# Performance work log

Hardware: AMD Instinct MI355X
Metric: run time of the kernel (lower is better)

The kernel has to match this reference:

```python
import jax, jax.numpy as jnp
import numpy as np

N = 20000   # nodes
E = 320000  # edges
F0 = 32     # num_features
H = 8       # GAT heads
G = 64      # graphs in batch


def setup_inputs() -> dict:
    key = jax.random.key(0)
    ks = jax.random.split(key, 16)
    def p(k, shape, s=0.05):
        return jax.random.normal(k, shape, jnp.float32) * s
    d = {}
    d['x'] = jax.random.normal(ks[0], (N, F0), jnp.float32)
    d['edge_index'] = jax.random.randint(ks[1], (2, E), 0, N, dtype=jnp.int32)
    d['edge_weights'] = jax.random.uniform(ks[2], (E,), jnp.float32)
    d['batch'] = jnp.sort(jax.random.randint(ks[3], (N,), 0, G, dtype=jnp.int32))
    # GATConv(32 -> 32, heads=8)
    d['W_gat'] = p(ks[4], (F0, H * F0)); d['att_src'] = p(ks[5], (H, F0))
    d['att_dst'] = p(ks[6], (H, F0));    d['b_gat'] = jnp.zeros((H * F0,), jnp.float32)
    # residual Linear(256 -> 1024) (widened so the residual add is shape-consistent)
    d['W_res'] = p(ks[7], (H * F0, 1024)); d['b_res'] = jnp.zeros((1024,), jnp.float32)
    # GCNConv(256 -> 512) + BN1
    d['W2'] = p(ks[8], (H * F0, 512)); d['b2'] = jnp.zeros((512,), jnp.float32)
    d['g1'] = jnp.ones((512,), jnp.float32); d['be1'] = jnp.zeros((512,), jnp.float32)
    d['m1'] = jnp.zeros((512,), jnp.float32); d['v1'] = jnp.ones((512,), jnp.float32)
    # GCNConv(512 -> 1024) + BN2
    d['W3'] = p(ks[9], (512, 1024)); d['b3'] = jnp.zeros((1024,), jnp.float32)
    d['g2'] = jnp.ones((1024,), jnp.float32); d['be2'] = jnp.zeros((1024,), jnp.float32)
    d['m2'] = jnp.zeros((1024,), jnp.float32); d['v2'] = jnp.ones((1024,), jnp.float32)
    # head
    d['Wf1'] = p(ks[10], (1024, 256)); d['bf1'] = jnp.zeros((256,), jnp.float32)
    d['Wf2'] = p(ks[11], (256, 2));    d['bf2'] = jnp.zeros((2,), jnp.float32)
    return d


def _add_self_loops(edge_index, edge_weight, n):
    loop = jnp.arange(n, dtype=edge_index.dtype)
    ei = jnp.concatenate([edge_index, jnp.stack([loop, loop])], axis=1)
    ew = jnp.concatenate([edge_weight, jnp.ones((n,), edge_weight.dtype)])
    return ei, ew


def _gat(x, edge_index, W, att_src, att_dst, b, n):
    # PyG GATConv, concat=True, eval (attention dropout off). Self-loops already added.
    src, dst = edge_index[0], edge_index[1]
    h = (x @ W).reshape(n, H, -1)                    # [N,H,C]
    a_s = jnp.einsum('nhc,hc->nh', h, att_src)        # [N,H]
    a_d = jnp.einsum('nhc,hc->nh', h, att_dst)
    e = jax.nn.leaky_relu(a_s[src] + a_d[dst], 0.2)   # [E,H]
    m = jax.ops.segment_max(e, dst, num_segments=n)   # softmax over incoming edges
    ex = jnp.exp(e - m[dst])
    s = jax.ops.segment_sum(ex, dst, num_segments=n)
    alpha = ex / s[dst]
    out = jax.ops.segment_sum(h[src] * alpha[:, :, None], dst, num_segments=n)
    return out.reshape(n, -1) + b                     # [N,H*C]


def _gcn(x, edge_index, w, W, b, n):
    # PyG GCNConv with symmetric normalization; self-loops (weight 1) already added.
    src, dst = edge_index[0], edge_index[1]
    deg = jax.ops.segment_sum(w, dst, num_segments=n)
    dinv = jnp.where(deg > 0, jax.lax.rsqrt(jnp.maximum(deg, 1e-12)), 0.0)
    norm = dinv[src] * w * dinv[dst]                  # [E]
    h = x @ W                                         # transform first (cheaper)
    return jax.ops.segment_sum(h[src] * norm[:, None], dst, num_segments=n) + b


def _bn(x, g, b, m, v):
    return g * (x - m) * jax.lax.rsqrt(v + 1e-5) + b


def reference(x, edge_index, edge_weights, batch, W_gat, att_src, att_dst, b_gat,
              W_res, b_res, W2, b2, g1, be1, m1, v1, W3, b3, g2, be2, m2, v2,
              Wf1, bf1, Wf2, bf2):
    n = x.shape[0]
    ei, ew = _add_self_loops(edge_index, edge_weights, n)
    h = jax.nn.relu(_gat(x, ei, W_gat, att_src, att_dst, b_gat, n))   # [N,256]
    res = h @ W_res + b_res                                           # [N,1024]
    h = _gcn(h, ei, ew, W2, b2, n)                                    # [N,512]
    h = jax.nn.relu(_bn(h, g1, be1, m1, v1))
    h = _gcn(h, ei, ew, W3, b3, n)                                    # [N,1024]
    h = jax.nn.relu(_bn(h, g2, be2, m2, v2))
    h = h + res
    pooled = jax.ops.segment_max(h, batch, num_segments=G)            # global max pool [G,1024]
    z = jax.nn.relu(pooled @ Wf1 + bf1)                               # dropout is eval no-op
    return z @ Wf2 + bf2                                              # [G,2]
```

## Files before the change

kernel.cpp:

```cpp
#include <hip/hip_runtime.h>
#include <hip/hip_bf16.h>

#define NN 20000
#define EE 320000
#define GG 64
#define EN (EE + NN)
#define MT 157

typedef float f32x4 __attribute__((ext_vector_type(4)));
typedef __bf16 bf16x4 __attribute__((ext_vector_type(4)));
typedef __bf16 bf16x8 __attribute__((ext_vector_type(8)));

__global__ void sentinel_kernel(float* out, int n) {
    int i = blockIdx.x * 256 + threadIdx.x;
    if (i < n) out[i] = 12345.0f;
}

__global__ void init_kernel(int* deg_cnt, float* deg_w, int* fill, float* pooled) {
    int i = blockIdx.x * 256 + threadIdx.x;
    if (i < NN) { deg_cnt[i] = 1; deg_w[i] = 1.0f; fill[i] = 0; }
    if (i < GG * 1024) pooled[i] = -INFINITY;
}

__global__ void convert_wt(const float* __restrict__ W, __bf16* __restrict__ Wt, int K, int N) {
    int n = blockIdx.x;
    for (int k = threadIdx.x; k < K; k += 256)
        Wt[(size_t)n * K + k] = (__bf16)W[(size_t)k * N + n];
}

__global__ __launch_bounds__(256) void gat_transform(
    const float* __restrict__ x, const float* __restrict__ W,
    const float* __restrict__ att_s, const float* __restrict__ att_d,
    __bf16* __restrict__ hlin, float* __restrict__ a_s, float* __restrict__ a_d)
{
    __shared__ float Ws[32 * 256];
    int tid = threadIdx.x;
#pragma unroll
    for (int k = 0; k < 32; k++) Ws[k * 256 + tid] = W[k * 256 + tid];
    float asc = att_s[tid], adc = att_d[tid];
    __syncthreads();
    for (int n = blockIdx.x; n < NN; n += gridDim.x) {
        const float* xp = x + (size_t)n * 32;
        float acc = 0.f;
#pragma unroll
        for (int k = 0; k < 32; k++) acc += xp[k] * Ws[k * 256 + tid];
        hlin[(size_t)n * 256 + tid] = (__bf16)acc;
        float s = acc * asc, d = acc * adc;
#pragma unroll
        for (int m = 1; m <= 16; m <<= 1) { s += __shfl_xor(s, m); d += __shfl_xor(d, m); }
        if ((tid & 31) == 0) { int h = tid >> 5; a_s[n * 8 + h] = s; a_d[n * 8 + h] = d; }
    }
}

__global__ void deg_kernel(const int* __restrict__ ei, const float* __restrict__ ew,
                           int* deg_cnt, float* deg_w) {
    int e = blockIdx.x * 256 + threadIdx.x;
    if (e >= EE) return;
    int dst = ei[EE + e];
    atomicAdd(&deg_cnt[dst], 1);
    atomicAdd(&deg_w[dst], ew[e]);
}

__global__ void dinv_kernel(const float* __restrict__ deg_w, float* __restrict__ dinv) {
    int n = blockIdx.x * 256 + threadIdx.x;
    if (n < NN) dinv[n] = rsqrtf(deg_w[n]);
}

__global__ __launch_bounds__(256) void scan_kernel(const int* __restrict__ deg_cnt, int* __restrict__ rowptr) {
    __shared__ int partial[256];
    int tid = threadIdx.x;
    const int chunk = (NN + 255) / 256;
    int s0 = tid * chunk, s1 = min(s0 + chunk, NN);
    int sum = 0;
    for (int i = s0; i < s1; i++) sum += deg_cnt[i];
    partial[tid] = sum;
    __syncthreads();
    if (tid == 0) {
        int run = 0;
        for (int i = 0; i < 256; i++) { int t = partial[i]; partial[i] = run; run += t; }
        rowptr[NN] = run;
    }
    __syncthreads();
    int run = partial[tid];
    for (int i = s0; i < s1; i++) { rowptr[i] = run; run += deg_cnt[i]; }
}

__global__ void fill_kernel(const int* __restrict__ ei, const float* __restrict__ ew,
                            const float* __restrict__ dinv, const int* __restrict__ rowptr,
                            int* fill, int* __restrict__ csr_src, float* __restrict__ csr_norm) {
    int e = blockIdx.x * 256 + threadIdx.x;
    if (e >= EN) return;
    int src, dst; float w;
    if (e < EE) { src = ei[e]; dst = ei[EE + e]; w = ew[e]; }
    else        { src = dst = e - EE; w = 1.0f; }
    int pos = atomicAdd(&fill[dst], 1);
    int slot = rowptr[dst] + pos;
    csr_src[slot] = src;
    csr_norm[slot] = dinv[src] * w * dinv[dst];
}

__global__ __launch_bounds__(256) void gat_agg(
    const int* __restrict__ rowptr, const int* __restrict__ csr_src,
    const float* __restrict__ a_s, const float* __restrict__ a_d,
    const __bf16* __restrict__ hlin, const float* __restrict__ b_gat,
    __bf16* __restrict__ h1)
{
    int widx = threadIdx.x >> 6, lane = threadIdx.x & 63;
    int node = blockIdx.x * 4 + widx;
    __shared__ int s_src[4][64];
    int base = rowptr[node], deg = rowptr[node + 1] - base;
    int hp1 = lane & 7, eslot = lane >> 3;
    float ad1 = a_d[node * 8 + hp1];
    float sum = 0.f;
    for (int e0 = 0; e0 < deg; e0 += 64) {
        int cnt = min(64, deg - e0);
        if (lane < cnt) s_src[widx][lane] = csr_src[base + e0 + lane];
        for (int s0 = 0; s0 < cnt; s0 += 8) {
            int e = s0 + eslot;
            if (e < cnt) {
                float v = a_s[s_src[widx][e] * 8 + hp1] + ad1;
                v = (v > 0.f) ? v : 0.2f * v;
                sum += __expf(v);
            }
        }
    }
#pragma unroll
    for (int m = 8; m <= 32; m <<= 1) sum += __shfl_xor(sum, m);
    int hp2 = lane >> 3;
    float sinv = 1.f / __shfl(sum, hp2);
    float ad2 = a_d[node * 8 + hp2];
    float acc[4] = {};
    for (int e0 = 0; e0 < deg; e0 += 64) {
        int cnt = min(64, deg - e0);
        if (lane < cnt) s_src[widx][lane] = csr_src[base + e0 + lane];
        for (int s = 0; s < cnt; s++) {
            int src = s_src[widx][s];
            float v = a_s[src * 8 + hp2] + ad2;
            v = (v > 0.f) ? v : 0.2f * v;
            float alpha = __expf(v) * sinv;
            bf16x4 f = *(const bf16x4*)(hlin + (size_t)src * 256 + lane * 4);
#pragma unroll
            for (int j = 0; j < 4; j++) acc[j] += alpha * (float)f[j];
        }
    }
    float4 bg = *(const float4*)(b_gat + lane * 4);
    bf16x4 o;
    o[0] = (__bf16)fmaxf(acc[0] + bg.x, 0.f);
    o[1] = (__bf16)fmaxf(acc[1] + bg.y, 0.f);
    o[2] = (__bf16)fmaxf(acc[2] + bg.z, 0.f);
    o[3] = (__bf16)fmaxf(acc[3] + bg.w, 0.f);
    *(bf16x4*)(h1 + (size_t)node * 256 + lane * 4) = o;
}

template <int C>
__global__ __launch_bounds__(256) void gcn_agg(
    const int* __restrict__ rowptr, const int* __restrict__ csr_src,
    const float* __restrict__ csr_norm, const __bf16* __restrict__ feat,
    __bf16* __restrict__ out)
{
    constexpr int V = C / 64;
    int widx = threadIdx.x >> 6, lane = threadIdx.x & 63;
    int node = blockIdx.x * 4 + widx;
    __shared__ int s_src[4][64];
    __shared__ float s_w[4][64];
    int base = rowptr[node], deg = rowptr[node + 1] - base;
    float acc[V];
#pragma unroll
    for (int j = 0; j < V; j++) acc[j] = 0.f;
    const __bf16* fb = feat + lane * V;
    for (int e0 = 0; e0 < deg; e0 += 64) {
        int cnt = min(64, deg - e0);
        if (lane < cnt) { s_src[widx][lane] = csr_src[base + e0 + lane]; s_w[widx][lane] = csr_norm[base + e0 + lane]; }
        for (int s = 0; s < cnt; s++) {
            int src = s_src[widx][s];
            float w = s_w[widx][s];
            if constexpr (V == 8) {
                bf16x8 f = *(const bf16x8*)(fb + (size_t)src * C);
#pragma unroll
                for (int j = 0; j < 8; j++) acc[j] += w * (float)f[j];
            } else {
                bf16x4 f = *(const bf16x4*)(fb + (size_t)src * C);
#pragma unroll
                for (int j = 0; j < 4; j++) acc[j] += w * (float)f[j];
            }
        }
    }
    if constexpr (V == 8) {
        bf16x8 o;
#pragma unroll
        for (int j = 0; j < 8; j++) o[j] = (__bf16)acc[j];
        *(bf16x8*)(out + (size_t)node * C + lane * V) = o;
    } else {
        bf16x4 o;
#pragma unroll
        for (int j = 0; j < 4; j++) o[j] = (__bf16)acc[j];
        *(bf16x4*)(out + (size_t)node * C + lane * V) = o;
    }
}

#define LSTR 40

__device__ __forceinline__ void stage_tiles(
    const __bf16* __restrict__ A, int K, const __bf16* __restrict__ Wt,
    int M, int bm, int bn, int k0, int tid, __bf16* As, __bf16* Bs)
{
#pragma unroll
    for (int i = 0; i < 2; i++) {
        int chunk = tid + i * 256;
        int r = chunk >> 2, c = chunk & 3;
        int gm = bm + r;
        bf16x8 v;
        if (gm < M) v = *(const bf16x8*)(A + (size_t)gm * K + k0 + c * 8);
        else {
#pragma unroll
            for (int j = 0; j < 8; j++) v[j] = (__bf16)0.f;
        }
        *(bf16x8*)(As + r * LSTR + c * 8) = v;
    }
#pragma unroll
    for (int i = 0; i < 2; i++) {
        int chunk = tid + i * 256;
        int n = chunk >> 2, c = chunk & 3;
        *(bf16x8*)(Bs + n * LSTR + c * 8) = *(const bf16x8*)(Wt + (size_t)(bn + n) * K + k0 + c * 8);
    }
}

__device__ __forceinline__ void mfma_step(
    const __bf16* As, const __bf16* Bs, int wr, int wc, int l16, int q, f32x4 (&acc)[4][4])
{
    bf16x8 af[4], bfv[4];
#pragma unroll
    for (int mt = 0; mt < 4; mt++) af[mt]  = *(const bf16x8*)(As + (wr * 64 + mt * 16 + l16) * LSTR + q * 8);
#pragma unroll
    for (int nt = 0; nt < 4; nt++) bfv[nt] = *(const bf16x8*)(Bs + (wc * 64 + nt * 16 + l16) * LSTR + q * 8);
#pragma unroll
    for (int mt = 0; mt < 4; mt++)
#pragma unroll
        for (int nt = 0; nt < 4; nt++)
            acc[mt][nt] = __builtin_amdgcn_mfma_f32_16x16x32_bf16(af[mt], bfv[nt], acc[mt][nt], 0, 0, 0);
}

__device__ __forceinline__ void gemm_loop(
    const __bf16* __restrict__ A, int K, const __bf16* __restrict__ Wt,
    int M, int bm, int bn, int tid, int wr, int wc, int l16, int q,
    __bf16* As, __bf16* Bs, f32x4 (&acc)[4][4])
{
    for (int k0 = 0; k0 < K; k0 += 32) {
        stage_tiles(A, K, Wt, M, bm, bn, k0, tid, As, Bs);
        __syncthreads();
        mfma_step(As, Bs, wr, wc, l16, q, acc);
        __syncthreads();
    }
}

__global__ __launch_bounds__(256) void gemm_bn_relu(
    const __bf16* __restrict__ A, const __bf16* __restrict__ Wt,
    int M, int K, int Nc,
    const float* __restrict__ bias,
    const float* __restrict__ g, const float* __restrict__ be,
    const float* __restrict__ mu, const float* __restrict__ var,
    __bf16* __restrict__ C)
{
    __shared__ __bf16 As[128 * LSTR];
    __shared__ __bf16 Bs[128 * LSTR];
    int tid = threadIdx.x;
    int w = tid >> 6, wr = w >> 1, wc = w & 1;
    int l = tid & 63, q = l >> 4, l16 = l & 15;
    int i = blockIdx.x;
    int k = (i & 3) * MT + (i >> 2);
    int bm = (k >> 2) * 128, bn = (k & 3) * 128;
    f32x4 acc[4][4] = {};
    gemm_loop(A, K, Wt, M, bm, bn, tid, wr, wc, l16, q, As, Bs, acc);
#pragma unroll
    for (int nt = 0; nt < 4; nt++) {
        int gn = bn + wc * 64 + nt * 16 + l16;
        float s = g[gn] * rsqrtf(var[gn] + 1e-5f);
        float t = be[gn] - mu[gn] * s;
        float bv = bias[gn];
#pragma unroll
        for (int mt = 0; mt < 4; mt++)
#pragma unroll
            for (int r = 0; r < 4; r++) {
                int gm = bm + wr * 64 + mt * 16 + q * 4 + r;
                if (gm < M) C[(size_t)gm * Nc + gn] = (__bf16)fmaxf((acc[mt][nt][r] + bv) * s + t, 0.f);
            }
    }
}

__device__ __forceinline__ void atomicMaxFloat(float* addr, float value) {
    if (value >= 0.f) atomicMax((int*)addr, __float_as_int(value));
    else              atomicMin((unsigned int*)addr, __float_as_uint(value));
}

__global__ __launch_bounds__(256) void gemm_final(
    const __bf16* __restrict__ A1, const __bf16* __restrict__ W3t,
    const __bf16* __restrict__ A2, const __bf16* __restrict__ Wrt,
    const float* __restrict__ b3, const float* __restrict__ bres,
    const float* __restrict__ g, const float* __restrict__ be,
    const float* __restrict__ mu, const float* __restrict__ var,
    const int* __restrict__ batch, float* __restrict__ pooled)
{
    const int M = NN;
    __shared__ __bf16 As[128 * LSTR];
    __shared__ __bf16 Bs[128 * LSTR];
    __shared__ int bat[128];
    int tid = threadIdx.x;
    int w = tid >> 6, wr = w >> 1, wc = w & 1;
    int l = tid & 63, q = l >> 4, l16 = l & 15;
    int i = blockIdx.x;
    int k = (i & 7) * MT + (i >> 3);
    int bm = (k >> 3) * 128, bn = (k & 7) * 128;
    if (tid < 128) bat[tid] = (bm + tid < M) ? batch[bm + tid] : -1;
    f32x4 acc[4][4] = {};
    f32x4 accR[4][4] = {};
    gemm_loop(A1, 512, W3t, M, bm, bn, tid, wr, wc, l16, q, As, Bs, acc);
    gemm_loop(A2, 256, Wrt, M, bm, bn, tid, wr, wc, l16, q, As, Bs, accR);
#pragma unroll
    for (int nt = 0; nt < 4; nt++) {
        int gn = bn + wc * 64 + nt * 16 + l16;
        float s = g[gn] * rsqrtf(var[gn] + 1e-5f);
        float t = be[gn] - mu[gn] * s;
        float bv3 = b3[gn];
        float bvr = bres[gn];
        int cb = -1; float run = 0.f;
#pragma unroll
        for (int mt = 0; mt < 4; mt++)
#pragma unroll
            for (int r = 0; r < 4; r++) {
                int lr = wr * 64 + mt * 16 + q * 4 + r;
                int id = bat[lr];
                if (id < 0) continue;
                float v = fmaxf((acc[mt][nt][r] + bv3) * s + t, 0.f) + accR[mt][nt][r] + bvr;
                if (id == cb) run = fmaxf(run, v);
                else {
                    if (cb >= 0) atomicMaxFloat(&pooled[cb * 1024 + gn], run);
                    cb = id; run = v;
                }
            }
        if (cb >= 0) atomicMaxFloat(&pooled[cb * 1024 + gn], run);
    }
}

__global__ __launch_bounds__(256) void head_kernel(
    const float* __restrict__ pooled, const float* __restrict__ Wf1, const float* __restrict__ bf1,
    const float* __restrict__ Wf2, const float* __restrict__ bf2, float* __restrict__ out)
{
    int gph = blockIdx.x, tid = threadIdx.x;
    __shared__ float prow[1024];
    __shared__ float zred[256];
    for (int i = tid; i < 1024; i += 256) prow[i] = pooled[gph * 1024 + i];
    __syncthreads();
    float z = 0.f;
    for (int k = 0; k < 1024; k++) z += prow[k] * Wf1[k * 256 + tid];
    z = fmaxf(z + bf1[tid], 0.f);
    for (int c = 0; c < 2; c++) {
        zred[tid] = z * Wf2[tid * 2 + c];
        __syncthreads();
        for (int s = 128; s > 0; s >>= 1) { if (tid < s) zred[tid] += zred[tid + s]; __syncthreads(); }
        if (tid == 0) out[gph * 2 + c] = zred[0] + bf2[c];
        __syncthreads();
    }
}

extern "C" void kernel_launch(void* const* d_in, const int* in_sizes, int n_in,
                              void* d_out, int out_size, void* d_ws, size_t ws_size,
                              hipStream_t stream) {
    const float* x       = (const float*)d_in[0];
    const int*   ei      = (const int*)d_in[1];
    const float* ew      = (const float*)d_in[2];
    const int*   batch   = (const int*)d_in[3];
    const float* W_gat   = (const float*)d_in[4];
    const float* att_src = (const float*)d_in[5];
    const float* att_dst = (const float*)d_in[6];
    const float* b_gat   = (const float*)d_in[7];
    const float* W_res   = (const float*)d_in[8];
    const float* b_res   = (const float*)d_in[9];
    const float* W2      = (const float*)d_in[10];
    const float* b2v     = (const float*)d_in[11];
    const float* g1      = (const float*)d_in[12];
    const float* be1     = (const float*)d_in[13];
    const float* m1      = (const float*)d_in[14];
    const float* v1      = (const float*)d_in[15];
    const float* W3      = (const float*)d_in[16];
    const float* b3      = (const float*)d_in[17];
    const float* g2      = (const float*)d_in[18];
    const float* be2     = (const float*)d_in[19];
    const float* m2      = (const float*)d_in[20];
    const float* v2      = (const float*)d_in[21];
    const float* Wf1     = (const float*)d_in[22];
    const float* bf1     = (const float*)d_in[23];
    const float* Wf2     = (const float*)d_in[24];
    const float* bf2v    = (const float*)d_in[25];
    float* out           = (float*)d_out;

    char* ws = (char*)d_ws;
    size_t off = 0;
    auto alloc = [&](size_t bytes) { size_t o = off; off += (bytes + 255) & ~(size_t)255; return o; };
    size_t o_hlin   = alloc((size_t)NN * 256 * 2);
    size_t o_h1     = alloc((size_t)NN * 256 * 2);
    size_t o_h2     = alloc((size_t)NN * 512 * 2);
    size_t o_agg2   = alloc((size_t)NN * 512 * 2);
    size_t o_as     = alloc((size_t)NN * 8 * 4);
    size_t o_ad     = alloc((size_t)NN * 8 * 4);
    size_t o_degc   = alloc((size_t)NN * 4);
    size_t o_degw   = alloc((size_t)NN * 4);
    size_t o_dinv   = alloc((size_t)NN * 4);
    size_t o_rowptr = alloc((size_t)(NN + 1) * 4);
    size_t o_fill   = alloc((size_t)NN * 4);
    size_t o_csrs   = alloc((size_t)EN * 4);
    size_t o_csrn   = alloc((size_t)EN * 4);
    size_t o_pool   = alloc((size_t)GG * 1024 * 4);
    size_t o_w2t    = alloc((size_t)512 * 256 * 2);
    size_t o_w3t    = alloc((size_t)1024 * 512 * 2);
    size_t o_wrt    = alloc((size_t)1024 * 256 * 2);
    if (off > ws_size) {
        sentinel_kernel<<<(out_size + 255) / 256, 256, 0, stream>>>(out, out_size);
        return;
    }

    __bf16* hlin   = (__bf16*)(ws + o_hlin);
    __bf16* agg1   = hlin;
    __bf16* h1     = (__bf16*)(ws + o_h1);
    __bf16* h2     = (__bf16*)(ws + o_h2);
    __bf16* agg2   = (__bf16*)(ws + o_agg2);
    float*  a_s    = (float*)(ws + o_as);
    float*  a_d    = (float*)(ws + o_ad);
    int*    degc   = (int*)(ws + o_degc);
    float*  degw   = (float*)(ws + o_degw);
    float*  dinv   = (float*)(ws + o_dinv);
    int*    rowptr = (int*)(ws + o_rowptr);
    int*    fillb  = (int*)(ws + o_fill);
    int*    csrs   = (int*)(ws + o_csrs);
    float*  csrn   = (float*)(ws + o_csrn);
    float*  pooled = (float*)(ws + o_pool);
    __bf16* W2t    = (__bf16*)(ws + o_w2t);
    __bf16* W3t    = (__bf16*)(ws + o_w3t);
    __bf16* Wrt    = (__bf16*)(ws + o_wrt);

    init_kernel<<<256, 256, 0, stream>>>(degc, degw, fillb, pooled);
    convert_wt<<<512, 256, 0, stream>>>(W2, W2t, 256, 512);
    convert_wt<<<1024, 256, 0, stream>>>(W3, W3t, 512, 1024);
    convert_wt<<<1024, 256, 0, stream>>>(W_res, Wrt, 256, 1024);

    gat_transform<<<512, 256, 0, stream>>>(x, W_gat, att_src, att_dst, hlin, a_s, a_d);
    deg_kernel<<<(EE + 255) / 256, 256, 0, stream>>>(ei, ew, degc, degw);
    dinv_kernel<<<(NN + 255) / 256, 256, 0, stream>>>(degw, dinv);
    scan_kernel<<<1, 256, 0, stream>>>(degc, rowptr);
    fill_kernel<<<(EN + 255) / 256, 256, 0, stream>>>(ei, ew, dinv, rowptr, fillb, csrs, csrn);
    gat_agg<<<NN / 4, 256, 0, stream>>>(rowptr, csrs, a_s, a_d, hlin, b_gat, h1);

    gcn_agg<256><<<NN / 4, 256, 0, stream>>>(rowptr, csrs, csrn, h1, agg1);
    gemm_bn_relu<<<4 * MT, 256, 0, stream>>>(agg1, W2t, NN, 256, 512, b2v,
        g1, be1, m1, v1, h2);
    gcn_agg<512><<<NN / 4, 256, 0, stream>>>(rowptr, csrs, csrn, h2, agg2);
    gemm_final<<<8 * MT, 256, 0, stream>>>(agg2, W3t, h1, Wrt,
        b3, b_res, g2, be2, m2, v2, batch, pooled);

    head_kernel<<<GG, 256, 0, stream>>>(pooled, Wf1, bf1, Wf2, bf2v, out);
}
```

Baseline: 465.8 us.

## Use async global-to-LDS GEMM loads, shuffle-based aggregation, single-pass GAT softmax

The GEMM tile staging now uses global_load_lds 16-byte async copies into an unpadded 32-wide LDS layout and drops the M bounds check. The GAT aggregation caches exp scores in registers for nodes with degree up to 64, so exponentials are computed once rather than twice. The GCN aggregation broadcasts edge indices and weights with wave shuffles instead of LDS. The separate dinv kernel is folded into fill_kernel via rsqrt. Risks: the last M tile reads past the end of the input rows, and the unpadded LDS layout may cause bank conflicts on the MFMA fragment reads.

```diff
diff --git a/kernel.cpp b/kernel.cpp
--- a/kernel.cpp
+++ b/kernel.cpp
@@ -10,6 +10,11 @@
 typedef float f32x4 __attribute__((ext_vector_type(4)));
 typedef __bf16 bf16x4 __attribute__((ext_vector_type(4)));
 typedef __bf16 bf16x8 __attribute__((ext_vector_type(8)));
+
+__device__ __forceinline__ void gl_lds16(const void* g, void* l) {
+    __builtin_amdgcn_global_load_lds((const __attribute__((address_space(1))) void*)g,
+                                     (__attribute__((address_space(3))) void*)l, 16, 0, 0);
+}
 
 __global__ void sentinel_kernel(float* out, int n) {
     int i = blockIdx.x * 256 + threadIdx.x;
@@ -59,11 +64,6 @@
     int dst = ei[EE + e];
     atomicAdd(&deg_cnt[dst], 1);
     atomicAdd(&deg_w[dst], ew[e]);
-}
-
-__global__ void dinv_kernel(const float* __restrict__ deg_w, float* __restrict__ dinv) {
-    int n = blockIdx.x * 256 + threadIdx.x;
-    if (n < NN) dinv[n] = rsqrtf(deg_w[n]);
 }
 
 __global__ __launch_bounds__(256) void scan_kernel(const int* __restrict__ deg_cnt, int* __restrict__ rowptr) {
@@ -86,7 +86,7 @@
 }
 
 __global__ void fill_kernel(const int* __restrict__ ei, const float* __restrict__ ew,
-                            const float* __restrict__ dinv, const int* __restrict__ rowptr,
+                            const float* __restrict__ deg_w, const int* __restrict__ rowptr,
                             int* fill, int* __restrict__ csr_src, float* __restrict__ csr_norm) {
     int e = blockIdx.x * 256 + threadIdx.x;
     if (e >= EN) return;
@@ -96,7 +96,7 @@
     int pos = atomicAdd(&fill[dst], 1);
     int slot = rowptr[dst] + pos;
     csr_src[slot] = src;
-    csr_norm[slot] = dinv[src] * w * dinv[dst];
+    csr_norm[slot] = rsqrtf(deg_w[src]) * w * rsqrtf(deg_w[dst]);
 }
 
 __global__ __launch_bounds__(256) void gat_agg(
@@ -107,40 +107,64 @@
 {
     int widx = threadIdx.x >> 6, lane = threadIdx.x & 63;
     int node = blockIdx.x * 4 + widx;
-    __shared__ int s_src[4][64];
     int base = rowptr[node], deg = rowptr[node + 1] - base;
-    int hp1 = lane & 7, eslot = lane >> 3;
-    float ad1 = a_d[node * 8 + hp1];
-    float sum = 0.f;
-    for (int e0 = 0; e0 < deg; e0 += 64) {
-        int cnt = min(64, deg - e0);
-        if (lane < cnt) s_src[widx][lane] = csr_src[base + e0 + lane];
-        for (int s0 = 0; s0 < cnt; s0 += 8) {
-            int e = s0 + eslot;
-            if (e < cnt) {
-                float v = a_s[s_src[widx][e] * 8 + hp1] + ad1;
-                v = (v > 0.f) ? v : 0.2f * v;
-                sum += __expf(v);
+    int hA = lane & 7;
+    int eslot = lane >> 3;
+    int hB = lane >> 3;
+    float adA = a_d[node * 8 + hA];
+    float acc[4] = {0.f, 0.f, 0.f, 0.f};
+
+    if (deg <= 64) {
+        int sv = (lane < deg) ? csr_src[base + lane] : 0;
+        float ev[8];
+        float psum = 0.f;
+#pragma unroll
+        for (int j = 0; j < 8; j++) {
+            int e = j * 8 + eslot;
+            float v = 0.f;
+            if (e < deg) {
+                int src = __shfl(sv, e);
+                float t = a_s[src * 8 + hA] + adA;
+                t = (t > 0.f) ? t : 0.2f * t;
+                v = __expf(t);
+            }
+            ev[j] = v;
+            psum += v;
+        }
+#pragma unroll
+        for (int m = 8; m <= 32; m <<= 1) psum += __shfl_xor(psum, m);
+        float sinv = 1.f / __shfl(psum, hB);
+#pragma unroll
+        for (int j = 0; j < 8; j++) {
+            if (j * 8 >= deg) break;
+            int lim = min(8, deg - j * 8);
+            for (int t = 0; t < lim; t++) {
+                int s = j * 8 + t;
+                int src = __shfl(sv, s);
+                float alpha = __shfl(ev[j], (t << 3) | hB) * sinv;
+                bf16x4 f = *(const bf16x4*)(hlin + (size_t)src * 256 + lane * 4);
+#pragma unroll
+                for (int c = 0; c < 4; c++) acc[c] += alpha * (float)f[c];
             }
         }
-    }
-#pragma unroll
-    for (int m = 8; m <= 32; m <<= 1) sum += __shfl_xor(sum, m);
-    int hp2 = lane >> 3;
-    float sinv = 1.f / __shfl(sum, hp2);
-    float ad2 = a_d[node * 8 + hp2];
-    float acc[4] = {};
-    for (int e0 = 0; e0 < deg; e0 += 64) {
-        int cnt = min(64, deg - e0);
-        if (lane < cnt) s_src[widx][lane] = csr_src[base + e0 + lane];
-        for (int s = 0; s < cnt; s++) {
-            int src = s_src[widx][s];
-            float v = a_s[src * 8 + hp2] + ad2;
-            v = (v > 0.f) ? v : 0.2f * v;
-            float alpha = __expf(v) * sinv;
+    } else {
+        float sum = 0.f;
+        for (int e = 0; e < deg; e++) {
+            int src = csr_src[base + e];
+            float t = a_s[src * 8 + hA] + adA;
+            t = (t > 0.f) ? t : 0.2f * t;
+            sum += __expf(t);
+        }
+        float sinv = 1.f / __shfl(sum, hB);
+        float adB = a_d[node * 8 + hB];
+        for (int e = 0; e < deg; e++) {
+            int src = csr_src[base + e];
+            float t = a_s[src * 8 + hB] + adB;
+            t = (t > 0.f) ? t : 0.2f * t;
+            float alpha = __expf(t) * sinv;
             bf16x4 f = *(const bf16x4*)(hlin + (size_t)src * 256 + lane * 4);
 #pragma unroll
-            for (int j = 0; j < 4; j++) acc[j] += alpha * (float)f[j];
+            for (int c = 0; c < 4; c++) acc[c] += alpha * (float)f[c];
         }
     }
     float4 bg = *(const float4*)(b_gat + lane * 4);
@@ -161,8 +185,6 @@
     constexpr int V = C / 64;
     int widx = threadIdx.x >> 6, lane = threadIdx.x & 63;
     int node = blockIdx.x * 4 + widx;
-    __shared__ int s_src[4][64];
-    __shared__ float s_w[4][64];
     int base = rowptr[node], deg = rowptr[node + 1] - base;
     float acc[V];
 #pragma unroll
@@ -170,10 +192,12 @@
     const __bf16* fb = feat + lane * V;
     for (int e0 = 0; e0 < deg; e0 += 64) {
         int cnt = min(64, deg - e0);
-        if (lane < cnt) { s_src[widx][lane] = csr_src[base + e0 + lane]; s_w[widx][lane] = csr_norm[base + e0 + lane]; }
+        int sv = 0; float wv = 0.f;
+        if (lane < cnt) { sv = csr_src[base + e0 + lane]; wv = csr_norm[base + e0 + lane]; }
+#pragma unroll 4
         for (int s = 0; s < cnt; s++) {
-            int src = s_src[widx][s];
-            float w = s_w[widx][s];
+            int src = __shfl(sv, s);
+            float w = __shfl(wv, s);
             if constexpr (V == 8) {
                 bf16x8 f = *(const bf16x8*)(fb + (size_t)src * C);
 #pragma unroll
@@ -198,30 +222,24 @@
     }
 }
 
-#define LSTR 40
-
-__device__ __forceinline__ void stage_tiles(
+
+__device__ __forceinline__ void stage_async(
     const __bf16* __restrict__ A, int K, const __bf16* __restrict__ Wt,
-    int M, int bm, int bn, int k0, int tid, __bf16* As, __bf16* Bs)
+    int bm, int bn, int k0, int tid, __bf16* As, __bf16* Bs)
 {
 #pragma unroll
     for (int i = 0; i < 2; i++) {
-        int chunk = tid + i * 256;
-        int r = chunk >> 2, c = chunk & 3;
-        int gm = bm + r;
-        bf16x8 v;
-        if (gm < M) v = *(const bf16x8*)(A + (size_t)gm * K + k0 + c * 8);
-        else {
-#pragma unroll
-            for (int j = 0; j < 8; j++) v[j] = (__bf16)0.f;
-        }
-        *(bf16x8*)(As + r * LSTR + c * 8) = v;
+        int j = i * 256 + tid;
+        int r = j >> 2, c = j & 3;
+        const __bf16* gp = A + (size_t)(bm + r) * K + k0 + c * 8;
+        gl_lds16(gp, As + (size_t)(j & ~63) * 8);
     }
 #pragma unroll
     for (int i = 0; i < 2; i++) {
-        int chunk = tid + i * 256;
-        int n = chunk >> 2, c = chunk & 3;
-        *(bf16x8*)(Bs + n * LSTR + c * 8) = *(const bf16x8*)(Wt + (size_t)(bn + n) * K + k0 + c * 8);
+        int j = i * 256 + tid;
+        int r = j >> 2, c = j & 3;
+        const __bf16* gp = Wt + (size_t)(bn + r) * K + k0 + c * 8;
+        gl_lds16(gp, Bs + (size_t)(j & ~63) * 8);
     }
 }
 
@@ -230,9 +248,9 @@
 {
     bf16x8 af[4], bfv[4];
 #pragma unroll
-    for (int mt = 0; mt < 4; mt++) af[mt]  = *(const bf16x8*)(As + (wr * 64 + mt * 16 + l16) * LSTR + q * 8);
-#pragma unroll
-    for (int nt = 0; nt < 4; nt++) bfv[nt] = *(const bf16x8*)(Bs + (wc * 64 + nt * 16 + l16) * LSTR + q * 8);
+    for (int mt = 0; mt < 4; mt++) af[mt]  = *(const bf16x8*)(As + (wr * 64 + mt * 16 + l16) * 32 + q * 8);
+#pragma unroll
+    for (int nt = 0; nt < 4; nt++) bfv[nt] = *(const bf16x8*)(Bs + (wc * 64 + nt * 16 + l16) * 32 + q * 8);
 #pragma unroll
     for (int mt = 0; mt < 4; mt++)
 #pragma unroll
@@ -242,11 +260,11 @@
 
 __device__ __forceinline__ void gemm_loop(
     const __bf16* __restrict__ A, int K, const __bf16* __restrict__ Wt,
-    int M, int bm, int bn, int tid, int wr, int wc, int l16, int q,
+    int bm, int bn, int tid, int wr, int wc, int l16, int q,
     __bf16* As, __bf16* Bs, f32x4 (&acc)[4][4])
 {
     for (int k0 = 0; k0 < K; k0 += 32) {
-        stage_tiles(A, K, Wt, M, bm, bn, k0, tid, As, Bs);
+        stage_async(A, K, Wt, bm, bn, k0, tid, As, Bs);
         __syncthreads();
         mfma_step(As, Bs, wr, wc, l16, q, acc);
         __syncthreads();
@@ -261,8 +279,8 @@
     const float* __restrict__ mu, const float* __restrict__ var,
     __bf16* __restrict__ C)
 {
-    __shared__ __bf16 As[128 * LSTR];
-    __shared__ __bf16 Bs[128 * LSTR];
+    __shared__ __bf16 As[128 * 32];
+    __shared__ __bf16 Bs[128 * 32];
     int tid = threadIdx.x;
     int w = tid >> 6, wr = w >> 1, wc = w & 1;
     int l = tid & 63, q = l >> 4, l16 = l & 15;
@@ -270,7 +288,7 @@
     int k = (i & 3) * MT + (i >> 2);
     int bm = (k >> 2) * 128, bn = (k & 3) * 128;
     f32x4 acc[4][4] = {};
-    gemm_loop(A, K, Wt, M, bm, bn, tid, wr, wc, l16, q, As, Bs, acc);
+    gemm_loop(A, K, Wt, bm, bn, tid, wr, wc, l16, q, As, Bs, acc);
 #pragma unroll
     for (int nt = 0; nt < 4; nt++) {
         int gn = bn + wc * 64 + nt * 16 + l16;
@@ -301,8 +319,8 @@
     const int* __restrict__ batch, float* __restrict__ pooled)
 {
     const int M = NN;
-    __shared__ __bf16 As[128 * LSTR];
-    __shared__ __bf16 Bs[128 * LSTR];
+    __shared__ __bf16 As[128 * 32];
+    __shared__ __bf16 Bs[128 * 32];
     __shared__ int bat[128];
     int tid = threadIdx.x;
     int w = tid >> 6, wr = w >> 1, wc = w & 1;
@@ -313,8 +331,8 @@
     if (tid < 128) bat[tid] = (bm + tid < M) ? batch[bm + tid] : -1;
     f32x4 acc[4][4] = {};
     f32x4 accR[4][4] = {};
-    gemm_loop(A1, 512, W3t, M, bm, bn, tid, wr, wc, l16, q, As, Bs, acc);
-    gemm_loop(A2, 256, Wrt, M, bm, bn, tid, wr, wc, l16, q, As, Bs, accR);
+    gemm_loop(A1, 512, W3t, bm, bn, tid, wr, wc, l16, q, As, Bs, acc);
+    gemm_loop(A2, 256, Wrt, bm, bn, tid, wr, wc, l16, q, As, Bs, accR);
 #pragma unroll
     for (int nt = 0; nt < 4; nt++) {
         int gn = bn + wc * 64 + nt * 16 + l16;
@@ -404,7 +422,6 @@
     size_t o_ad     = alloc((size_t)NN * 8 * 4);
     size_t o_degc   = alloc((size_t)NN * 4);
     size_t o_degw   = alloc((size_t)NN * 4);
-    size_t o_dinv   = alloc((size_t)NN * 4);
     size_t o_rowptr = alloc((size_t)(NN + 1) * 4);
     size_t o_fill   = alloc((size_t)NN * 4);
     size_t o_csrs   = alloc((size_t)EN * 4);
@@ -427,7 +444,6 @@
     float*  a_d    = (float*)(ws + o_ad);
     int*    degc   = (int*)(ws + o_degc);
     float*  degw   = (float*)(ws + o_degw);
-    float*  dinv   = (float*)(ws + o_dinv);
     int*    rowptr = (int*)(ws + o_rowptr);
     int*    fillb  = (int*)(ws + o_fill);
     int*    csrs   = (int*)(ws + o_csrs);
@@ -444,9 +460,8 @@
 
     gat_transform<<<512, 256, 0, stream>>>(x, W_gat, att_src, att_dst, hlin, a_s, a_d);
     deg_kernel<<<(EE + 255) / 256, 256, 0, stream>>>(ei, ew, degc, degw);
-    dinv_kernel<<<(NN + 255) / 256, 256, 0, stream>>>(degw, dinv);
     scan_kernel<<<1, 256, 0, stream>>>(degc, rowptr);
-    fill_kernel<<<(EN + 255) / 256, 256, 0, stream>>>(ei, ew, dinv, rowptr, fillb, csrs, csrn);
+    fill_kernel<<<(EN + 255) / 256, 256, 0, stream>>>(ei, ew, degw, rowptr, fillb, csrs, csrn);
     gat_agg<<<NN / 4, 256, 0, stream>>>(rowptr, csrs, a_s, a_d, hlin, b_gat, h1);
 
     gcn_agg<256><<<NN / 4, 256, 0, stream>>>(rowptr, csrs, csrn, h1, agg1);
```

Measured after the change: 465.3 us. No clear change (-0.1%).
